# Optimization experiments

Measured on AMD Instinct MI355X. Metric: run time of the kernel, lower is better.

The kernel has to match this reference:

```python
import jax, jax.numpy as jnp
import numpy as np

HID = 128
OUT = 64
LAYERS = 2
N_ACT, N_RS, N_RD = 100000, 20000, 50000
E_F, E_RS, E_RD, E_HRD = 1600000, 800000, 800000, 800000
NEG_SLOPE = 0.2  # PyG GATConv default


def setup_inputs() -> dict:
    key = jax.random.key(0)
    k = jax.random.split(key, 20)
    s = 1.0 / np.sqrt(HID)
    inp = {
        "x_act": jax.random.normal(k[0], (N_ACT, HID), jnp.float32),
        "x_rs": jax.random.normal(k[1], (N_RS, HID), jnp.float32),
        "x_rd": jax.random.normal(k[2], (N_RD, HID), jnp.float32),
        "ef_src": jax.random.randint(k[3], (E_F,), 0, N_ACT, jnp.int32),
        "ef_dst": jax.random.randint(k[4], (E_F,), 0, N_ACT, jnp.int32),
        "ers_src": jax.random.randint(k[5], (E_RS,), 0, N_ACT, jnp.int32),
        "ers_dst": jax.random.randint(k[6], (E_RS,), 0, N_RS, jnp.int32),
        "erd_src": jax.random.randint(k[7], (E_RD,), 0, N_RD, jnp.int32),
        "erd_dst": jax.random.randint(k[8], (E_RD,), 0, N_RD, jnp.int32),
        "ehrd_src": jax.random.randint(k[9], (E_HRD,), 0, N_ACT, jnp.int32),
        "ehrd_dst": jax.random.randint(k[10], (E_HRD,), 0, N_RD, jnp.int32),
        # GAT params stacked [n_rel=4, layers=2, ...]; rel order: follows, has_rs, rd_delta, has_rd
        "Wsrc": jax.random.normal(k[11], (4, LAYERS, HID, HID), jnp.float32) * s,
        "Wdst": jax.random.normal(k[12], (4, LAYERS, HID, HID), jnp.float32) * s,
        "att_src": jax.random.normal(k[13], (4, LAYERS, HID), jnp.float32) * s,
        "att_dst": jax.random.normal(k[14], (4, LAYERS, HID), jnp.float32) * s,
        "b_gat": jnp.zeros((4, LAYERS, HID), jnp.float32),
        "W_ln": jax.random.normal(k[15], (HID, HID), jnp.float32) * s,
        "b_ln": jnp.zeros((HID,), jnp.float32),
        "W_fc": jax.random.normal(k[16], (HID, OUT), jnp.float32) * s,
        "b_fc": jnp.zeros((OUT,), jnp.float32),
    }
    return inp


def _gat(x_src, x_dst, src, dst, Ws, Wd, a_s, a_d, b):
    """Single-head PyG GATConv (add_self_loops=False), bipartite."""
    n_dst = x_dst.shape[0]
    hs = x_src @ Ws                       # [Nsrc, HID]
    hd = x_dst @ Wd                       # [Ndst, HID]
    e = jax.nn.leaky_relu((hs @ a_s)[src] + (hd @ a_d)[dst], NEG_SLOPE)  # [E]
    m = jax.ops.segment_max(e, dst, num_segments=n_dst)
    m = jnp.where(jnp.isfinite(m), m, 0.0)  # empty segments -> harmless 0
    p = jnp.exp(e - m[dst])
    z = jax.ops.segment_sum(p, dst, num_segments=n_dst)
    w = p / jnp.maximum(z, 1e-16)[dst]    # segment softmax over incoming edges
    out = jax.ops.segment_sum(w[:, None] * hs[src], dst, num_segments=n_dst)
    return out + b


def reference(x_act, x_rs, x_rd, ef_src, ef_dst, ers_src, ers_dst, erd_src, erd_dst,
              ehrd_src, ehrd_dst, Wsrc, Wdst, att_src, att_dst, b_gat,
              W_ln, b_ln, W_fc, b_fc):
    xa, xrs, xrd = x_act, x_rs, x_rd
    for L in range(LAYERS):
        a_new = _gat(xa, xa, ef_src, ef_dst, Wsrc[0, L], Wdst[0, L],
                     att_src[0, L], att_dst[0, L], b_gat[0, L])
        rs_new = _gat(xa, xrs, ers_src, ers_dst, Wsrc[1, L], Wdst[1, L],
                      att_src[1, L], att_dst[1, L], b_gat[1, L])
        # HeteroConv aggr='sum': resource_dynamic gets two conv outputs summed
        rd_new = (_gat(xrd, xrd, erd_src, erd_dst, Wsrc[2, L], Wdst[2, L],
                       att_src[2, L], att_dst[2, L], b_gat[2, L])
                  + _gat(xa, xrd, ehrd_src, ehrd_dst, Wsrc[3, L], Wdst[3, L],
                         att_src[3, L], att_dst[3, L], b_gat[3, L]))
        xa, xrs, xrd = jax.nn.relu(a_new), jax.nn.relu(rs_new), jax.nn.relu(rd_new)
    feats = jnp.stack([jnp.mean(jax.nn.relu(x @ W_ln + b_ln), axis=0)
                       for x in (xa, xrs, xrd)])  # [3, HID]
    pooled = jnp.mean(feats, axis=0)
    return pooled @ W_fc + b_fc  # [OUT]
```

## Files before the change

### kernel.cpp

```cpp
#include <hip/hip_runtime.h>
#include <cmath>

#define HID 128

typedef __attribute__((ext_vector_type(8))) short bf16x8;
typedef __attribute__((ext_vector_type(4))) float f32x4;

__device__ inline unsigned short f2bf_rne(float f) {
  unsigned int b = __float_as_uint(f);
  return (unsigned short)((b + 0x7fffu + ((b >> 16) & 1u)) >> 16);
}
__device__ inline float bf2f(unsigned int u) { return __uint_as_float(u << 16); }

#define NDTOT 220000
#define ETOT 4000000
#define BSH 8
#define BDST 256
#define NB 860
#define EPB 16384
#define NBINBLK 245


__global__ void fill_f_kernel(float* p, float v, int n) {
  int i = blockIdx.x * 256 + threadIdx.x;
  if (i < n) p[i] = v;
}

__global__ void fill_i_kernel(int* p, int v, int n) {
  int i = blockIdx.x * 256 + threadIdx.x;
  if (i < n) p[i] = v;
}

__global__ void f2bf_kernel(const float* __restrict__ in, unsigned short* __restrict__ out,
                            int n8) {
  int i = blockIdx.x * 256 + threadIdx.x;
  if (i >= n8) return;
  const float4* p4 = reinterpret_cast<const float4*>(in) + (size_t)i * 2;
  float4 v0 = p4[0], v1 = p4[1];
  float vv[8] = {v0.x, v0.y, v0.z, v0.w, v1.x, v1.y, v1.z, v1.w};
  unsigned int r[8];
#pragma unroll
  for (int j = 0; j < 8; ++j) r[j] = f2bf_rne(vv[j]);
  uint4 o;
  o.x = r[0] | (r[1] << 16);
  o.y = r[2] | (r[3] << 16);
  o.z = r[4] | (r[5] << 16);
  o.w = r[6] | (r[7] << 16);
  reinterpret_cast<uint4*>(out)[i] = o;
}

__global__ void pack_w_kernel(const float* __restrict__ Wsrc8, const float* __restrict__ W_ln,
                              unsigned short* __restrict__ Wp) {
  int g = blockIdx.y;
  const float* W = (g < 8) ? (Wsrc8 + (size_t)g * 16384) : W_ln;
  unsigned short* op = Wp + (size_t)g * 16384;
  int o = blockIdx.x * 256 + threadIdx.x;
  if (o >= 16384) return;
  int j = o & 7;
  int lane = (o >> 3) & 63;
  int kk = (o >> 9) & 3;
  int ct = (o >> 11) & 3;
  int half = (o >> 13) & 1;
  int k = kk * 32 + ((lane >> 4) * 8) + j;
  int col = half * 64 + ct * 16 + (lane & 15);
  op[o] = f2bf_rne(W[k * 128 + col]);
}

__global__ void compute_v_kernel(const float* __restrict__ W, const float* __restrict__ a,
                                 float* __restrict__ v) {
  int g = blockIdx.x, k = threadIdx.x;
  const float* Wg = W + g * 16384;
  const float* ag = a + g * 128;
  float s = 0.f;
  for (int c = 0; c < 128; ++c) s = fmaf(Wg[k * 128 + c], ag[c], s);
  v[g * 128 + k] = s;
}

__device__ inline const float* pick_vec(int r, const float* vs, const float* vd, int L) {
  switch (r) {
    case 0: return vs + (0 + L) * 128;
    case 1: return vd + (0 + L) * 128;
    case 2: return vs + (2 + L) * 128;
    case 3: return vs + (6 + L) * 128;
    case 4: return vs + (4 + L) * 128;
    case 5: return vd + (4 + L) * 128;
    case 6: return vd + (6 + L) * 128;
    default: return vd + (2 + L) * 128;
  }
}

__global__ __launch_bounds__(256) void matvec_fused_kernel(
    const unsigned short* __restrict__ xa, const unsigned short* __restrict__ xrd,
    const unsigned short* __restrict__ xrs, const float* __restrict__ vs,
    const float* __restrict__ vd, int L, float* __restrict__ af_s, float* __restrict__ af_d,
    float* __restrict__ ars_s, float* __restrict__ ahrd_s, float* __restrict__ ard_s,
    float* __restrict__ ard_d, float* __restrict__ ahrd_d, float* __restrict__ ars_d) {
  __shared__ float vl[11][128];
  int tid = threadIdx.x;
  for (int i = tid; i < 1024; i += 256) {
    int r = i >> 7;
    vl[r][i & 127] = pick_vec(r, vs, vd, L)[i & 127];
  }
  for (int i = tid; i < 384; i += 256) vl[8 + (i >> 7)][i & 127] = 0.f;
  __syncthreads();
  int wave = tid >> 6, lane = tid & 63;
  int sub = lane >> 4, li = lane & 15;
  int row = blockIdx.x * 16 + wave * 4 + sub;
  if (row >= 170000) return;
  const unsigned short* X; int lrow, vbase;
  if (row < 100000)      { X = xa;  lrow = row;          vbase = 0; }
  else if (row < 150000) { X = xrd; lrow = row - 100000; vbase = 4; }
  else                   { X = xrs; lrow = row - 150000; vbase = 7; }
  const uint4 xv = *reinterpret_cast<const uint4*>(X + (size_t)lrow * 128 + li * 8);
  float f[8];
  f[0] = bf2f(xv.x & 0xffffu); f[1] = bf2f(xv.x >> 16);
  f[2] = bf2f(xv.y & 0xffffu); f[3] = bf2f(xv.y >> 16);
  f[4] = bf2f(xv.z & 0xffffu); f[5] = bf2f(xv.z >> 16);
  f[6] = bf2f(xv.w & 0xffffu); f[7] = bf2f(xv.w >> 16);
  float a0 = 0.f, a1 = 0.f, a2 = 0.f, a3 = 0.f;
#pragma unroll
  for (int q = 0; q < 8; ++q) {
    int col = li * 8 + q;
    a0 = fmaf(f[q], vl[vbase][col], a0);
    a1 = fmaf(f[q], vl[vbase + 1][col], a1);
    a2 = fmaf(f[q], vl[vbase + 2][col], a2);
    a3 = fmaf(f[q], vl[vbase + 3][col], a3);
  }
#pragma unroll
  for (int off = 8; off >= 1; off >>= 1) {
    a0 += __shfl_xor(a0, off);
    a1 += __shfl_xor(a1, off);
    a2 += __shfl_xor(a2, off);
    a3 += __shfl_xor(a3, off);
  }
  if (li == 0) {
    if (row < 100000) {
      af_s[lrow] = a0; af_d[lrow] = a1; ars_s[lrow] = a2; ahrd_s[lrow] = a3;
    } else if (row < 150000) {
      ard_s[lrow] = a0; ard_d[lrow] = a1; ahrd_d[lrow] = a2;
    } else {
      ars_d[lrow] = a0;
    }
  }
}

__global__ void max4_kernel(const float* __restrict__ a0, const float* __restrict__ a1,
                            const float* __restrict__ a2, const float* __restrict__ a3,
                            int n0, int n1, int n2, int n3, unsigned int* __restrict__ outm) {
  int y = blockIdx.y;
  const float* a = (y == 0) ? a0 : (y == 1) ? a1 : (y == 2) ? a2 : a3;
  int n = (y == 0) ? n0 : (y == 1) ? n1 : (y == 2) ? n2 : n3;
  float m = 0.f;
  for (int i = blockIdx.x * 256 + threadIdx.x; i < n; i += gridDim.x * 256)
    m = fmaxf(m, fabsf(a[i]));
#pragma unroll
  for (int off = 32; off >= 1; off >>= 1) m = fmaxf(m, __shfl_xor(m, off));
  if ((threadIdx.x & 63) == 0) atomicMax(&outm[y], __float_as_uint(m));
}


__device__ inline void decode_edge(int e, const int* __restrict__ s0, const int* __restrict__ d0,
                                   const int* __restrict__ s1, const int* __restrict__ d1,
                                   const int* __restrict__ s2, const int* __restrict__ d2,
                                   const int* __restrict__ s3, const int* __restrict__ d3,
                                   int& src, int& gd) {
  const int* sp; const int* dp; int base, doff;
  if (e < 1600000)      { sp = s0; dp = d0; base = 0;       doff = 0; }
  else if (e < 2400000) { sp = s1; dp = d1; base = 1600000; doff = 100000; }
  else if (e < 3200000) { sp = s2; dp = d2; base = 2400000; doff = 120000; }
  else                  { sp = s3; dp = d3; base = 3200000; doff = 170000; }
  int i = e - base;
  src = sp[i];
  gd = doff + dp[i];
}

__global__ __launch_bounds__(256) void bin_hist_kernel(
    const int* __restrict__ d0, const int* __restrict__ d1, const int* __restrict__ d2,
    const int* __restrict__ d3, int* __restrict__ bcnt) {
  __shared__ int lh[NB];
  for (int i = threadIdx.x; i < NB; i += 256) lh[i] = 0;
  __syncthreads();
  int e0 = blockIdx.x * EPB;
  for (int i = 0; i < EPB; i += 256) {
    int e = e0 + i + threadIdx.x;
    if (e < ETOT) {
      const int* dp; int base, doff;
      if (e < 1600000)      { dp = d0; base = 0;       doff = 0; }
      else if (e < 2400000) { dp = d1; base = 1600000; doff = 100000; }
      else if (e < 3200000) { dp = d2; base = 2400000; doff = 120000; }
      else                  { dp = d3; base = 3200000; doff = 170000; }
      atomicAdd(&lh[(doff + dp[e - base]) >> BSH], 1);
    }
  }
  __syncthreads();
  for (int i = threadIdx.x; i < NB; i += 256)
    if (lh[i]) atomicAdd(&bcnt[i], lh[i]);
}

__global__ void scan_nb_kernel(const int* __restrict__ bcnt, int* __restrict__ bbase) {
  if (threadIdx.x == 0 && blockIdx.x == 0) {
    int run = 0;
    for (int b = 0; b < NB; ++b) { bbase[b] = run; run += bcnt[b]; }
    bbase[NB] = run;
  }
}

__global__ __launch_bounds__(256) void bin_scatter_kernel(
    const int* __restrict__ s0, const int* __restrict__ d0, const int* __restrict__ s1,
    const int* __restrict__ d1, const int* __restrict__ s2, const int* __restrict__ d2,
    const int* __restrict__ s3, const int* __restrict__ d3, const int* __restrict__ bbase,
    int* __restrict__ bfill, int2* __restrict__ pair_buf) {
  __shared__ int lh[NB];
  __shared__ int lbase[NB];
  for (int i = threadIdx.x; i < NB; i += 256) lh[i] = 0;
  __syncthreads();
  int e0 = blockIdx.x * EPB;
  for (int i = 0; i < EPB; i += 256) {
    int e = e0 + i + threadIdx.x;
    if (e < ETOT) {
      const int* dp; int base, doff;
      if (e < 1600000)      { dp = d0; base = 0;       doff = 0; }
      else if (e < 2400000) { dp = d1; base = 1600000; doff = 100000; }
      else if (e < 3200000) { dp = d2; base = 2400000; doff = 120000; }
      else                  { dp = d3; base = 3200000; doff = 170000; }
      atomicAdd(&lh[(doff + dp[e - base]) >> BSH], 1);
    }
  }
  __syncthreads();
  for (int i = threadIdx.x; i < NB; i += 256) {
    int c = lh[i];
    if (c) lbase[i] = bbase[i] + atomicAdd(&bfill[i], c);
    lh[i] = 0;
  }
  __syncthreads();
  for (int i = 0; i < EPB; i += 256) {
    int e = e0 + i + threadIdx.x;
    if (e < ETOT) {
      int src, gd;
      decode_edge(e, s0, d0, s1, d1, s2, d2, s3, d3, src, gd);
      int b = gd >> BSH;
      int pos = atomicAdd(&lh[b], 1);
      pair_buf[lbase[b] + pos] = make_int2(src, gd);
    }
  }
}

__global__ __launch_bounds__(256) void bucket_build_kernel(
    const int2* __restrict__ pair_buf, const int* __restrict__ bbase,
    int* __restrict__ rowptr_cat, int* __restrict__ csr_cat) {
  __shared__ int lcnt[BDST];
  __shared__ int lrp[BDST + 1];
  int b = blockIdx.x;
  int d0 = b << BSH;
  int nd = min(BDST, NDTOT - d0);
  int base = bbase[b], end = bbase[b + 1];
  for (int i = threadIdx.x; i < nd; i += 256) lcnt[i] = 0;
  __syncthreads();
  for (int j = base + threadIdx.x; j < end; j += 256)
    atomicAdd(&lcnt[pair_buf[j].y - d0], 1);
  __syncthreads();
  if (threadIdx.x == 0) {
    int run = base;
    for (int i = 0; i < nd; ++i) { lrp[i] = run; run += lcnt[i]; }
    lrp[nd] = run;
  }
  __syncthreads();
  for (int i = threadIdx.x; i <= nd; i += 256) rowptr_cat[d0 + i] = lrp[i];
  for (int i = threadIdx.x; i < nd; i += 256) lcnt[i] = 0;
  __syncthreads();
  for (int j = base + threadIdx.x; j < end; j += 256) {
    int2 pr = pair_buf[j];
    int ld = pr.y - d0;
    int pos = lrp[ld] + atomicAdd(&lcnt[ld], 1);
    csr_cat[pos] = pr.x;
  }
}

#define ACC8(xv, wgt)                                   \
  do {                                                  \
    a[0] = fmaf(wgt, bf2f((xv).x & 0xffffu), a[0]);     \
    a[1] = fmaf(wgt, bf2f((xv).x >> 16), a[1]);         \
    a[2] = fmaf(wgt, bf2f((xv).y & 0xffffu), a[2]);     \
    a[3] = fmaf(wgt, bf2f((xv).y >> 16), a[3]);         \
    a[4] = fmaf(wgt, bf2f((xv).z & 0xffffu), a[4]);     \
    a[5] = fmaf(wgt, bf2f((xv).z >> 16), a[5]);         \
    a[6] = fmaf(wgt, bf2f((xv).w & 0xffffu), a[6]);     \
    a[7] = fmaf(wgt, bf2f((xv).w >> 16), a[7]);         \
  } while (0)

__global__ __launch_bounds__(256) void gat_aggr_fused(
    const int* __restrict__ rowptr_cat, const int* __restrict__ csr_cat,
    const float* __restrict__ af_s, const float* __restrict__ af_d,
    const float* __restrict__ ars_s, const float* __restrict__ ars_d,
    const float* __restrict__ ard_s, const float* __restrict__ ard_d,
    const float* __restrict__ ahrd_s, const float* __restrict__ ahrd_d,
    const unsigned int* __restrict__ asmax, const unsigned short* __restrict__ xa,
    const unsigned short* __restrict__ xrd, unsigned short* __restrict__ aggh) {
  __shared__ float2 sp[4][64];
  int wave = threadIdx.x >> 6, lane = threadIdx.x & 63;
  int g = lane >> 4, li = lane & 15;
  int gd = blockIdx.x * 4 + wave;
  if (gd >= NDTOT) return;
  const float* as_; const float* ad_; const unsigned short* Xh; int midx, d;
  if (gd < 100000)      { as_ = af_s;  ad_ = af_d;  Xh = xa;  midx = 0; d = gd; }
  else if (gd < 120000) { as_ = ars_s; ad_ = ars_d; Xh = xa;  midx = 1; d = gd - 100000; }
  else if (gd < 170000) { as_ = ard_s; ad_ = ard_d; Xh = xrd; midx = 3; d = gd - 120000; }
  else                  { as_ = ahrd_s; ad_ = ahrd_d; Xh = xa; midx = 2; d = gd - 170000; }
  int beg = rowptr_cat[gd], end = rowptr_cat[gd + 1];
  float ad = ad_[d];
  float t0 = __uint_as_float(asmax[midx]) + ad;
  float mh = t0 > 0.f ? t0 : 0.2f * t0;
  float z = 0.f;
  float a[8] = {};
  for (int c0 = beg; c0 < end; c0 += 64) {
    int j = c0 + lane;
    int s = 0;
    float p = 0.f;
    if (j < end) {
      s = csr_cat[j];
      float t = as_[s] + ad;
      float e = t > 0.f ? t : 0.2f * t;
      p = __expf(e - mh);
      z += p;
    }
    sp[wave][lane] = make_float2(__int_as_float(s), p);
    asm volatile("s_waitcnt lgkmcnt(0)" ::: "memory");
    int cnt = min(64, end - c0);
    for (int k = g; k < cnt; k += 16) {
      float2 w0 = sp[wave][k];
      float2 w1 = (k + 4 < cnt) ? sp[wave][k + 4] : make_float2(0.f, 0.f);
      float2 w2 = (k + 8 < cnt) ? sp[wave][k + 8] : make_float2(0.f, 0.f);
      float2 w3 = (k + 12 < cnt) ? sp[wave][k + 12] : make_float2(0.f, 0.f);
      const uint4 x0 = *reinterpret_cast<const uint4*>(
          Xh + (size_t)(unsigned)__float_as_int(w0.x) * 128 + li * 8);
      const uint4 x1 = *reinterpret_cast<const uint4*>(
          Xh + (size_t)(unsigned)__float_as_int(w1.x) * 128 + li * 8);
      const uint4 x2 = *reinterpret_cast<const uint4*>(
          Xh + (size_t)(unsigned)__float_as_int(w2.x) * 128 + li * 8);
      const uint4 x3 = *reinterpret_cast<const uint4*>(
          Xh + (size_t)(unsigned)__float_as_int(w3.x) * 128 + li * 8);
      ACC8(x0, w0.y);
      ACC8(x1, w1.y);
      ACC8(x2, w2.y);
      ACC8(x3, w3.y);
    }
  }
#pragma unroll
  for (int off = 32; off >= 1; off >>= 1) z += __shfl_xor(z, off);
#pragma unroll
  for (int i = 0; i < 8; ++i) {
    a[i] += __shfl_xor(a[i], 32);
    a[i] += __shfl_xor(a[i], 16);
  }
  if (g == 0) {
    float inv = 1.f / fmaxf(z, 1e-16f);
    uint4 o;
    o.x = (unsigned)f2bf_rne(a[0] * inv) | ((unsigned)f2bf_rne(a[1] * inv) << 16);
    o.y = (unsigned)f2bf_rne(a[2] * inv) | ((unsigned)f2bf_rne(a[3] * inv) << 16);
    o.z = (unsigned)f2bf_rne(a[4] * inv) | ((unsigned)f2bf_rne(a[5] * inv) << 16);
    o.w = (unsigned)f2bf_rne(a[6] * inv) | ((unsigned)f2bf_rne(a[7] * inv) << 16);
    *reinterpret_cast<uint4*>(aggh + (size_t)gd * 128 + li * 8) = o;
  }
}

__global__ __launch_bounds__(256) void gemm_all_kernel(
    const unsigned short* __restrict__ aggh, const unsigned short* __restrict__ wpack,
    const float* __restrict__ b_gat, int L, unsigned short* __restrict__ ya,
    unsigned short* __restrict__ yrs, unsigned short* __restrict__ yrd) {
  int bx = blockIdx.x;
  const unsigned short *X1, *X2 = nullptr, *Wp1, *Wp2 = nullptr;
  const float *bias1, *bias2 = nullptr;
  unsigned short* Y;
  int N, r0;
  if (bx < 782) {
    int gg = 0 + L;
    X1 = aggh; Wp1 = wpack + (size_t)gg * 16384; bias1 = b_gat + gg * 128;
    Y = ya; N = 100000; r0 = bx * 128;
  } else if (bx < 939) {
    int gg = 2 + L;
    X1 = aggh + (size_t)100000 * 128; Wp1 = wpack + (size_t)gg * 16384;
    bias1 = b_gat + gg * 128;
    Y = yrs; N = 20000; r0 = (bx - 782) * 128;
  } else {
    int g2 = 4 + L, g3 = 6 + L;
    X1 = aggh + (size_t)120000 * 128; Wp1 = wpack + (size_t)g2 * 16384;
    bias1 = b_gat + g2 * 128;
    X2 = aggh + (size_t)170000 * 128; Wp2 = wpack + (size_t)g3 * 16384;
    bias2 = b_gat + g3 * 128;
    Y = yrd; N = 50000; r0 = (bx - 939) * 128;
  }
  int wid = threadIdx.x >> 6, lane = threadIdx.x & 63;
  int half = blockIdx.y;
  int rr0 = r0 + wid * 32;
  int lr = lane & 15, gk = lane >> 4;
  f32x4 acc[2][4];
#pragma unroll
  for (int rt = 0; rt < 2; ++rt)
#pragma unroll
    for (int ct = 0; ct < 4; ++ct) acc[rt][ct] = (f32x4){0.f, 0.f, 0.f, 0.f};
  int row0 = rr0 + lr, row1 = rr0 + 16 + lr;
  int nph = X2 ? 2 : 1;
  for (int ph = 0; ph < nph; ++ph) {
    const unsigned short* X = ph ? X2 : X1;
    const unsigned short* Wp = ph ? Wp2 : Wp1;
    bf16x8 b[4][4];
#pragma unroll
    for (int ct = 0; ct < 4; ++ct)
#pragma unroll
      for (int kk = 0; kk < 4; ++kk)
        b[ct][kk] = *reinterpret_cast<const bf16x8*>(Wp + ((((half * 4 + ct) * 4 + kk) * 64 + lane) << 3));
#pragma unroll
    for (int kk = 0; kk < 4; ++kk) {
      bf16x8 a0 = {}, a1 = {};
      if (row0 < N) a0 = *reinterpret_cast<const bf16x8*>(X + (size_t)row0 * 128 + kk * 32 + gk * 8);
      if (row1 < N) a1 = *reinterpret_cast<const bf16x8*>(X + (size_t)row1 * 128 + kk * 32 + gk * 8);
#pragma unroll
      for (int ct = 0; ct < 4; ++ct) {
        acc[0][ct] = __builtin_amdgcn_mfma_f32_16x16x32_bf16(a0, b[ct][kk], acc[0][ct], 0, 0, 0);
        acc[1][ct] = __builtin_amdgcn_mfma_f32_16x16x32_bf16(a1, b[ct][kk], acc[1][ct], 0, 0, 0);
      }
    }
  }
#pragma unroll
  for (int rt = 0; rt < 2; ++rt)
#pragma unroll
    for (int ct = 0; ct < 4; ++ct) {
      int col = half * 64 + ct * 16 + lr;
      float bcol = bias1[col] + (bias2 ? bias2[col] : 0.f);
#pragma unroll
      for (int reg = 0; reg < 4; ++reg) {
        int row = rr0 + rt * 16 + gk * 4 + reg;
        if (row < N) {
          float o = acc[rt][ct][reg] + bcol;
          Y[(size_t)row * 128 + col] = f2bf_rne(fmaxf(o, 0.f));
        }
      }
    }
}

__global__ __launch_bounds__(256) void head_fused_kernel(
    const unsigned short* __restrict__ xa, const unsigned short* __restrict__ xrs,
    const unsigned short* __restrict__ xrd, const unsigned short* __restrict__ Wp,
    const float* __restrict__ bias, float* __restrict__ feat) {
  __shared__ float cs[64];
  int bx = blockIdx.x;
  const unsigned short* X; float* f; int N, bx0;
  if (bx < 196)      { X = xa;  f = feat;       N = 100000; bx0 = bx; }
  else if (bx < 236) { X = xrs; f = feat + 128; N = 20000;  bx0 = bx - 196; }
  else               { X = xrd; f = feat + 256; N = 50000;  bx0 = bx - 236; }
  int wid = threadIdx.x >> 6, lane = threadIdx.x & 63;
  int half = blockIdx.y;
  int lr = lane & 15, gk = lane >> 4;
  if (threadIdx.x < 64) cs[threadIdx.x] = 0.f;
  __syncthreads();
  bf16x8 b[4][4];
#pragma unroll
  for (int ct = 0; ct < 4; ++ct)
#pragma unroll
    for (int kk = 0; kk < 4; ++kk)
      b[ct][kk] = *reinterpret_cast<const bf16x8*>(Wp + ((((half * 4 + ct) * 4 + kk) * 64 + lane) << 3));
  float colsum[4] = {0.f, 0.f, 0.f, 0.f};
  for (int c = 0; c < 4; ++c) {
    int r0 = bx0 * 512 + c * 128 + wid * 32;
    if (r0 >= N) break;
    f32x4 acc[2][4];
#pragma unroll
    for (int rt = 0; rt < 2; ++rt)
#pragma unroll
      for (int ct = 0; ct < 4; ++ct) acc[rt][ct] = (f32x4){0.f, 0.f, 0.f, 0.f};
    int row0 = r0 + lr, row1 = r0 + 16 + lr;
#pragma unroll
    for (int kk = 0; kk < 4; ++kk) {
      bf16x8 a0 = {}, a1 = {};
      if (row0 < N) a0 = *reinterpret_cast<const bf16x8*>(X + (size_t)row0 * 128 + kk * 32 + gk * 8);
      if (row1 < N) a1 = *reinterpret_cast<const bf16x8*>(X + (size_t)row1 * 128 + kk * 32 + gk * 8);
#pragma unroll
      for (int ct = 0; ct < 4; ++ct) {
        acc[0][ct] = __builtin_amdgcn_mfma_f32_16x16x32_bf16(a0, b[ct][kk], acc[0][ct], 0, 0, 0);
        acc[1][ct] = __builtin_amdgcn_mfma_f32_16x16x32_bf16(a1, b[ct][kk], acc[1][ct], 0, 0, 0);
      }
    }
#pragma unroll
    for (int rt = 0; rt < 2; ++rt)
#pragma unroll
      for (int ct = 0; ct < 4; ++ct) {
        float bcol = bias[half * 64 + ct * 16 + lr];
#pragma unroll
        for (int reg = 0; reg < 4; ++reg) {
          int row = r0 + rt * 16 + gk * 4 + reg;
          if (row < N) colsum[ct] += fmaxf(acc[rt][ct][reg] + bcol, 0.f);
        }
      }
  }
#pragma unroll
  for (int ct = 0; ct < 4; ++ct) {
    float v = colsum[ct];
    v += __shfl_xor(v, 16);
    v += __shfl_xor(v, 32);
    if (gk == 0) atomicAdd(&cs[ct * 16 + lr], v);
  }
  __syncthreads();
  if (threadIdx.x < 64) atomicAdd(&f[half * 64 + threadIdx.x], cs[threadIdx.x]);
}

__global__ void final_fc_kernel(const float* __restrict__ fa, const float* __restrict__ frs,
                                const float* __restrict__ frd, const float* __restrict__ Wfc,
                                const float* __restrict__ bfc, float* __restrict__ out) {
  __shared__ float pooled[128];
  int t = threadIdx.x;
  if (t < 128)
    pooled[t] = (fa[t] * (1.f / 100000.f) + frs[t] * (1.f / 20000.f) + frd[t] * (1.f / 50000.f)) *
                (1.f / 3.f);
  __syncthreads();
  if (t < 64) {
    float s = bfc[t];
    for (int c = 0; c < 128; ++c) s = fmaf(pooled[c], Wfc[c * 64 + t], s);
    out[t] = s;
  }
}


extern "C" void kernel_launch(void* const* d_in, const int* in_sizes, int n_in,
                              void* d_out, int out_size, void* d_ws, size_t ws_size,
                              hipStream_t stream) {
  const int N_ACT = 100000, N_RS = 20000, N_RD = 50000;

  const float* x_act = (const float*)d_in[0];
  const float* x_rs = (const float*)d_in[1];
  const float* x_rd = (const float*)d_in[2];
  const int* ef_src = (const int*)d_in[3];
  const int* ef_dst = (const int*)d_in[4];
  const int* ers_src = (const int*)d_in[5];
  const int* ers_dst = (const int*)d_in[6];
  const int* erd_src = (const int*)d_in[7];
  const int* erd_dst = (const int*)d_in[8];
  const int* ehrd_src = (const int*)d_in[9];
  const int* ehrd_dst = (const int*)d_in[10];
  const float* Wsrc = (const float*)d_in[11];
  const float* Wdst = (const float*)d_in[12];
  const float* att_src = (const float*)d_in[13];
  const float* att_dst = (const float*)d_in[14];
  const float* b_gat = (const float*)d_in[15];
  const float* W_ln = (const float*)d_in[16];
  const float* b_ln = (const float*)d_in[17];
  const float* W_fc = (const float*)d_in[18];
  const float* b_fc = (const float*)d_in[19];
  float* out = (float*)d_out;

  float* w = (float*)d_ws;
  float* af_s = w;   w += N_ACT;
  float* af_d = w;   w += N_ACT;
  float* ars_s = w;  w += N_ACT;
  float* ahrd_s = w; w += N_ACT;
  float* ard_s = w;  w += N_RD;
  float* ard_d = w;  w += N_RD;
  float* ahrd_d = w; w += N_RD;
  float* ars_d = w;  w += N_RS;
  float* vs = w;    w += 1024;
  float* vd = w;    w += 1024;
  float* feats = w; w += 384;
  unsigned int* asmax_u = (unsigned int*)w; w += 16;
  unsigned short* xa0 = (unsigned short*)w;   w += (size_t)N_ACT * 64;
  unsigned short* xa1 = (unsigned short*)w;   w += (size_t)N_ACT * 64;
  unsigned short* xrd0 = (unsigned short*)w;  w += (size_t)N_RD * 64;
  unsigned short* xrd1 = (unsigned short*)w;  w += (size_t)N_RD * 64;
  unsigned short* xrs_b = (unsigned short*)w; w += (size_t)N_RS * 64;
  unsigned short* aggh = (unsigned short*)w;  w += (size_t)NDTOT * 64;
  unsigned short* wpack = (unsigned short*)w; w += (9 * 16384) / 2;
  int* ip = (int*)w;
  int2* pair_buf = (int2*)ip; ip += 2 * ETOT;
  int* csr_cat = ip;          ip += ETOT;
  int* rowptr_cat = ip;       ip += NDTOT + 1;
  int* bcnt = ip;             ip += NB;
  int* bfill = ip;            ip += NB;
  int* bbase = ip;            ip += NB + 1;

  fill_i_kernel<<<(2 * NB + 255) / 256, 256, 0, stream>>>(bcnt, 0, 2 * NB);
  bin_hist_kernel<<<NBINBLK, 256, 0, stream>>>(ef_dst, ers_dst, erd_dst, ehrd_dst, bcnt);
  scan_nb_kernel<<<1, 64, 0, stream>>>(bcnt, bbase);
  bin_scatter_kernel<<<NBINBLK, 256, 0, stream>>>(
      ef_src, ef_dst, ers_src, ers_dst, erd_src, erd_dst, ehrd_src, ehrd_dst,
      bbase, bfill, pair_buf);
  bucket_build_kernel<<<NB, 256, 0, stream>>>(pair_buf, bbase, rowptr_cat, csr_cat);

  compute_v_kernel<<<8, 128, 0, stream>>>(Wsrc, att_src, vs);
  compute_v_kernel<<<8, 128, 0, stream>>>(Wdst, att_dst, vd);
  pack_w_kernel<<<dim3(64, 9), 256, 0, stream>>>(Wsrc, W_ln, wpack);
  f2bf_kernel<<<(N_ACT * 16 + 255) / 256, 256, 0, stream>>>(x_act, xa0, N_ACT * 16);
  f2bf_kernel<<<(N_RS * 16 + 255) / 256, 256, 0, stream>>>(x_rs, xrs_b, N_RS * 16);
  f2bf_kernel<<<(N_RD * 16 + 255) / 256, 256, 0, stream>>>(x_rd, xrd0, N_RD * 16);

  const unsigned short* xa = xa0;
  unsigned short* xa_nxt = xa1;
  const unsigned short* xrd = xrd0;
  unsigned short* xrd_nxt = xrd1;

  for (int L = 0; L < 2; ++L) {
    matvec_fused_kernel<<<(170000 + 15) / 16, 256, 0, stream>>>(
        xa, xrd, xrs_b, vs, vd, L, af_s, af_d, ars_s, ahrd_s, ard_s, ard_d, ahrd_d, ars_d);

    fill_i_kernel<<<1, 64, 0, stream>>>((int*)asmax_u, 0, 16);
    max4_kernel<<<dim3(32, 4), 256, 0, stream>>>(af_s, ars_s, ahrd_s, ard_s,
                                                 N_ACT, N_ACT, N_ACT, N_RD, asmax_u);

    gat_aggr_fused<<<(NDTOT + 3) / 4, 256, 0, stream>>>(
        rowptr_cat, csr_cat, af_s, af_d, ars_s, ars_d, ard_s, ard_d, ahrd_s, ahrd_d,
        asmax_u, xa, xrd, aggh);

    gemm_all_kernel<<<dim3(1330, 2), 256, 0, stream>>>(aggh, wpack, b_gat, L,
                                                       xa_nxt, xrs_b, xrd_nxt);

    const unsigned short* t1 = xa; xa = xa_nxt; xa_nxt = (unsigned short*)t1;
    const unsigned short* t2 = xrd; xrd = xrd_nxt; xrd_nxt = (unsigned short*)t2;
  }

  fill_f_kernel<<<2, 256, 0, stream>>>(feats, 0.f, 384);
  head_fused_kernel<<<dim3(334, 2), 256, 0, stream>>>(xa, xrs_b, xrd,
                                                      wpack + (size_t)8 * 16384, b_ln, feats);
  final_fc_kernel<<<1, 128, 0, stream>>>(feats, feats + 128, feats + 256, W_fc, b_fc, out);
}
```

Measured before the change: 624.9 us.

## Merge small setup kernels and unroll GAT aggregation with packed FMA

Several small launches are merged: the three bf16 conversions become one kernel, the two attention-vector kernels become one 2D launch, and the max-reduction now also zeroes feats, which removes the separate fill launches. The max kernel changes from 128 blocks with atomics to 4 blocks with float4 loads and a shared-memory reduction, so each block has more serial work. The aggregation loop is unrolled to 8 gathers per iteration. It uses byte-offset indices pre-shifted by 8, reads padded zero entries in shared memory instead of bounds checks, and accumulates with v_pk_fma_f32 inline asm to raise memory-level parallelism and cut ALU instructions.

```diff
diff --git a/kernel.cpp b/kernel.cpp
--- a/kernel.cpp
+++ b/kernel.cpp
@@ -5,6 +5,7 @@
 
 typedef __attribute__((ext_vector_type(8))) short bf16x8;
 typedef __attribute__((ext_vector_type(4))) float f32x4;
+typedef __attribute__((ext_vector_type(2))) float f32x2;
 
 __device__ inline unsigned short f2bf_rne(float f) {
   unsigned int b = __float_as_uint(f);
@@ -21,21 +22,21 @@
 #define NBINBLK 245
 
 
-__global__ void fill_f_kernel(float* p, float v, int n) {
-  int i = blockIdx.x * 256 + threadIdx.x;
-  if (i < n) p[i] = v;
-}
-
 __global__ void fill_i_kernel(int* p, int v, int n) {
   int i = blockIdx.x * 256 + threadIdx.x;
   if (i < n) p[i] = v;
 }
 
-__global__ void f2bf_kernel(const float* __restrict__ in, unsigned short* __restrict__ out,
-                            int n8) {
+__global__ void f2bf_all_kernel(const float* __restrict__ xa, const float* __restrict__ xrs,
+                                const float* __restrict__ xrd, unsigned short* __restrict__ oa,
+                                unsigned short* __restrict__ ors, unsigned short* __restrict__ ord) {
   int i = blockIdx.x * 256 + threadIdx.x;
-  if (i >= n8) return;
-  const float4* p4 = reinterpret_cast<const float4*>(in) + (size_t)i * 2;
+  const float* in; unsigned short* out; int li;
+  if (i < 1600000)      { in = xa;  out = oa;  li = i; }
+  else if (i < 1920000) { in = xrs; out = ors; li = i - 1600000; }
+  else if (i < 2720000) { in = xrd; out = ord; li = i - 1920000; }
+  else return;
+  const float4* p4 = reinterpret_cast<const float4*>(in) + (size_t)li * 2;
   float4 v0 = p4[0], v1 = p4[1];
   float vv[8] = {v0.x, v0.y, v0.z, v0.w, v1.x, v1.y, v1.z, v1.w};
   unsigned int r[8];
@@ -46,7 +47,7 @@
   o.y = r[2] | (r[3] << 16);
   o.z = r[4] | (r[5] << 16);
   o.w = r[6] | (r[7] << 16);
-  reinterpret_cast<uint4*>(out)[i] = o;
+  reinterpret_cast<uint4*>(out)[li] = o;
 }
 
 __global__ void pack_w_kernel(const float* __restrict__ Wsrc8, const float* __restrict__ W_ln,
@@ -66,14 +67,16 @@
   op[o] = f2bf_rne(W[k * 128 + col]);
 }
 
-__global__ void compute_v_kernel(const float* __restrict__ W, const float* __restrict__ a,
-                                 float* __restrict__ v) {
+__global__ void compute_v2_kernel(const float* __restrict__ Wsrc, const float* __restrict__ Wdst,
+                                  const float* __restrict__ as_, const float* __restrict__ ad_,
+                                  float* __restrict__ vs, float* __restrict__ vd) {
   int g = blockIdx.x, k = threadIdx.x;
-  const float* Wg = W + g * 16384;
-  const float* ag = a + g * 128;
+  const float* W = (blockIdx.y ? Wdst : Wsrc) + g * 16384;
+  const float* a = (blockIdx.y ? ad_ : as_) + g * 128;
+  float* v = (blockIdx.y ? vd : vs) + g * 128;
   float s = 0.f;
-  for (int c = 0; c < 128; ++c) s = fmaf(Wg[k * 128 + c], ag[c], s);
-  v[g * 128 + k] = s;
+  for (int c = 0; c < 128; ++c) s = fmaf(W[k * 128 + c], a[c], s);
+  v[k] = s;
 }
 
 __device__ inline const float* pick_vec(int r, const float* vs, const float* vd, int L) {
@@ -144,18 +147,29 @@
   }
 }
 
-__global__ void max4_kernel(const float* __restrict__ a0, const float* __restrict__ a1,
-                            const float* __restrict__ a2, const float* __restrict__ a3,
-                            int n0, int n1, int n2, int n3, unsigned int* __restrict__ outm) {
-  int y = blockIdx.y;
+__global__ __launch_bounds__(256) void max4_kernel(
+    const float* __restrict__ a0, const float* __restrict__ a1, const float* __restrict__ a2,
+    const float* __restrict__ a3, int n0, int n1, int n2, int n3,
+    unsigned int* __restrict__ outm, float* feats_zero) {
+  __shared__ float red[256];
+  int y = blockIdx.x, tid = threadIdx.x;
+  if (feats_zero && y == 0)
+    for (int i = tid; i < 384; i += 256) feats_zero[i] = 0.f;
   const float* a = (y == 0) ? a0 : (y == 1) ? a1 : (y == 2) ? a2 : a3;
-  int n = (y == 0) ? n0 : (y == 1) ? n1 : (y == 2) ? n2 : n3;
+  int n4 = ((y == 0) ? n0 : (y == 1) ? n1 : (y == 2) ? n2 : n3) >> 2;
   float m = 0.f;
-  for (int i = blockIdx.x * 256 + threadIdx.x; i < n; i += gridDim.x * 256)
-    m = fmaxf(m, fabsf(a[i]));
-#pragma unroll
-  for (int off = 32; off >= 1; off >>= 1) m = fmaxf(m, __shfl_xor(m, off));
-  if ((threadIdx.x & 63) == 0) atomicMax(&outm[y], __float_as_uint(m));
+  const float4* a4 = reinterpret_cast<const float4*>(a);
+  for (int i = tid; i < n4; i += 256) {
+    float4 v = a4[i];
+    m = fmaxf(m, fmaxf(fmaxf(fabsf(v.x), fabsf(v.y)), fmaxf(fabsf(v.z), fabsf(v.w))));
+  }
+  red[tid] = m;
+  __syncthreads();
+  for (int off = 128; off; off >>= 1) {
+    if (tid < off) red[tid] = fmaxf(red[tid], red[tid + off]);
+    __syncthreads();
+  }
+  if (tid == 0) outm[y] = __float_as_uint(red[0]);
 }
 
 
@@ -276,16 +290,17 @@
   }
 }
 
-#define ACC8(xv, wgt)                                   \
-  do {                                                  \
-    a[0] = fmaf(wgt, bf2f((xv).x & 0xffffu), a[0]);     \
-    a[1] = fmaf(wgt, bf2f((xv).x >> 16), a[1]);         \
-    a[2] = fmaf(wgt, bf2f((xv).y & 0xffffu), a[2]);     \
-    a[3] = fmaf(wgt, bf2f((xv).y >> 16), a[3]);         \
-    a[4] = fmaf(wgt, bf2f((xv).z & 0xffffu), a[4]);     \
-    a[5] = fmaf(wgt, bf2f((xv).z >> 16), a[5]);         \
-    a[6] = fmaf(wgt, bf2f((xv).w & 0xffffu), a[6]);     \
-    a[7] = fmaf(wgt, bf2f((xv).w >> 16), a[7]);         \
+#define ACCP(xv, wgt)                                                                \
+  do {                                                                               \
+    f32x2 wv = {wgt, wgt};                                                           \
+    f32x2 t0 = {__uint_as_float((xv).x << 16), __uint_as_float((xv).x & 0xFFFF0000u)};\
+    f32x2 t1 = {__uint_as_float((xv).y << 16), __uint_as_float((xv).y & 0xFFFF0000u)};\
+    f32x2 t2 = {__uint_as_float((xv).z << 16), __uint_as_float((xv).z & 0xFFFF0000u)};\
+    f32x2 t3 = {__uint_as_float((xv).w << 16), __uint_as_float((xv).w & 0xFFFF0000u)};\
+    asm("v_pk_fma_f32 %0, %1, %2, %0" : "+v"(a2[0]) : "v"(wv), "v"(t0));             \
+    asm("v_pk_fma_f32 %0, %1, %2, %0" : "+v"(a2[1]) : "v"(wv), "v"(t1));             \
+    asm("v_pk_fma_f32 %0, %1, %2, %0" : "+v"(a2[2]) : "v"(wv), "v"(t2));             \
+    asm("v_pk_fma_f32 %0, %1, %2, %0" : "+v"(a2[3]) : "v"(wv), "v"(t3));             \
   } while (0)
 
 __global__ __launch_bounds__(256) void gat_aggr_fused(
@@ -296,7 +311,7 @@
     const float* __restrict__ ahrd_s, const float* __restrict__ ahrd_d,
     const unsigned int* __restrict__ asmax, const unsigned short* __restrict__ xa,
     const unsigned short* __restrict__ xrd, unsigned short* __restrict__ aggh) {
-  __shared__ float2 sp[4][64];
+  __shared__ float2 sp[4][96];
   int wave = threadIdx.x >> 6, lane = threadIdx.x & 63;
   int g = lane >> 4, li = lane & 15;
   int gd = blockIdx.x * 4 + wave;
@@ -306,45 +321,57 @@
   else if (gd < 120000) { as_ = ars_s; ad_ = ars_d; Xh = xa;  midx = 1; d = gd - 100000; }
   else if (gd < 170000) { as_ = ard_s; ad_ = ard_d; Xh = xrd; midx = 3; d = gd - 120000; }
   else                  { as_ = ahrd_s; ad_ = ahrd_d; Xh = xa; midx = 2; d = gd - 170000; }
+  if (lane < 32) sp[wave][64 + lane] = make_float2(0.f, 0.f);
+  const char* Xb = reinterpret_cast<const char*>(Xh) + li * 16;
   int beg = rowptr_cat[gd], end = rowptr_cat[gd + 1];
   float ad = ad_[d];
-  float t0 = __uint_as_float(asmax[midx]) + ad;
-  float mh = t0 > 0.f ? t0 : 0.2f * t0;
+  float t0v = __uint_as_float(asmax[midx]) + ad;
+  float mh = t0v > 0.f ? t0v : 0.2f * t0v;
   float z = 0.f;
-  float a[8] = {};
+  f32x2 a2[4] = {{0.f, 0.f}, {0.f, 0.f}, {0.f, 0.f}, {0.f, 0.f}};
   for (int c0 = beg; c0 < end; c0 += 64) {
     int j = c0 + lane;
-    int s = 0;
+    int s8 = 0;
     float p = 0.f;
     if (j < end) {
-      s = csr_cat[j];
+      int s = csr_cat[j];
       float t = as_[s] + ad;
       float e = t > 0.f ? t : 0.2f * t;
       p = __expf(e - mh);
       z += p;
-    }
-    sp[wave][lane] = make_float2(__int_as_float(s), p);
+      s8 = s << 8;
+    }
+    sp[wave][lane] = make_float2(__int_as_float(s8), p);
     asm volatile("s_waitcnt lgkmcnt(0)" ::: "memory");
     int cnt = min(64, end - c0);
-    for (int k = g; k < cnt; k += 16) {
+    for (int k = g; k < cnt; k += 32) {
       float2 w0 = sp[wave][k];
-      float2 w1 = (k + 4 < cnt) ? sp[wave][k + 4] : make_float2(0.f, 0.f);
-      float2 w2 = (k + 8 < cnt) ? sp[wave][k + 8] : make_float2(0.f, 0.f);
-      float2 w3 = (k + 12 < cnt) ? sp[wave][k + 12] : make_float2(0.f, 0.f);
-      const uint4 x0 = *reinterpret_cast<const uint4*>(
-          Xh + (size_t)(unsigned)__float_as_int(w0.x) * 128 + li * 8);
-      const uint4 x1 = *reinterpret_cast<const uint4*>(
-          Xh + (size_t)(unsigned)__float_as_int(w1.x) * 128 + li * 8);
-      const uint4 x2 = *reinterpret_cast<const uint4*>(
-          Xh + (size_t)(unsigned)__float_as_int(w2.x) * 128 + li * 8);
-      const uint4 x3 = *reinterpret_cast<const uint4*>(
-          Xh + (size_t)(unsigned)__float_as_int(w3.x) * 128 + li * 8);
-      ACC8(x0, w0.y);
-      ACC8(x1, w1.y);
-      ACC8(x2, w2.y);
-      ACC8(x3, w3.y);
-    }
-  }
+      float2 w1 = sp[wave][k + 4];
+      float2 w2 = sp[wave][k + 8];
+      float2 w3 = sp[wave][k + 12];
+      float2 w4 = sp[wave][k + 16];
+      float2 w5 = sp[wave][k + 20];
+      float2 w6 = sp[wave][k + 24];
+      float2 w7 = sp[wave][k + 28];
+      const uint4 x0 = *reinterpret_cast<const uint4*>(Xb + (unsigned)__float_as_int(w0.x));
+      const uint4 x1 = *reinterpret_cast<const uint4*>(Xb + (unsigned)__float_as_int(w1.x));
+      const uint4 x2 = *reinterpret_cast<const uint4*>(Xb + (unsigned)__float_as_int(w2.x));
+      const uint4 x3 = *reinterpret_cast<const uint4*>(Xb + (unsigned)__float_as_int(w3.x));
+      const uint4 x4 = *reinterpret_cast<const uint4*>(Xb + (unsigned)__float_as_int(w4.x));
+      const uint4 x5 = *reinterpret_cast<const uint4*>(Xb + (unsigned)__float_as_int(w5.x));
+      const uint4 x6 = *reinterpret_cast<const uint4*>(Xb + (unsigned)__float_as_int(w6.x));
+      const uint4 x7 = *reinterpret_cast<const uint4*>(Xb + (unsigned)__float_as_int(w7.x));
+      ACCP(x0, w0.y);
+      ACCP(x1, w1.y);
+      ACCP(x2, w2.y);
+      ACCP(x3, w3.y);
+      ACCP(x4, w4.y);
+      ACCP(x5, w5.y);
+      ACCP(x6, w6.y);
+      ACCP(x7, w7.y);
+    }
+  }
+  float a[8] = {a2[0].x, a2[0].y, a2[1].x, a2[1].y, a2[2].x, a2[2].y, a2[3].x, a2[3].y};
 #pragma unroll
   for (int off = 32; off >= 1; off >>= 1) z += __shfl_xor(z, off);
 #pragma unroll
@@ -583,12 +610,10 @@
       bbase, bfill, pair_buf);
   bucket_build_kernel<<<NB, 256, 0, stream>>>(pair_buf, bbase, rowptr_cat, csr_cat);
 
-  compute_v_kernel<<<8, 128, 0, stream>>>(Wsrc, att_src, vs);
-  compute_v_kernel<<<8, 128, 0, stream>>>(Wdst, att_dst, vd);
+  compute_v2_kernel<<<dim3(8, 2), 128, 0, stream>>>(Wsrc, Wdst, att_src, att_dst, vs, vd);
   pack_w_kernel<<<dim3(64, 9), 256, 0, stream>>>(Wsrc, W_ln, wpack);
-  f2bf_kernel<<<(N_ACT * 16 + 255) / 256, 256, 0, stream>>>(x_act, xa0, N_ACT * 16);
-  f2bf_kernel<<<(N_RS * 16 + 255) / 256, 256, 0, stream>>>(x_rs, xrs_b, N_RS * 16);
-  f2bf_kernel<<<(N_RD * 16 + 255) / 256, 256, 0, stream>>>(x_rd, xrd0, N_RD * 16);
+  f2bf_all_kernel<<<(2720000 + 255) / 256, 256, 0, stream>>>(x_act, x_rs, x_rd,
+                                                             xa0, xrs_b, xrd0);
 
   const unsigned short* xa = xa0;
   unsigned short* xa_nxt = xa1;
@@ -599,9 +624,9 @@
     matvec_fused_kernel<<<(170000 + 15) / 16, 256, 0, stream>>>(
         xa, xrd, xrs_b, vs, vd, L, af_s, af_d, ars_s, ahrd_s, ard_s, ard_d, ahrd_d, ars_d);
 
-    fill_i_kernel<<<1, 64, 0, stream>>>((int*)asmax_u, 0, 16);
-    max4_kernel<<<dim3(32, 4), 256, 0, stream>>>(af_s, ars_s, ahrd_s, ard_s,
-                                                 N_ACT, N_ACT, N_ACT, N_RD, asmax_u);
+    max4_kernel<<<4, 256, 0, stream>>>(af_s, ars_s, ahrd_s, ard_s,
+                                       N_ACT, N_ACT, N_ACT, N_RD, asmax_u,
+                                       (L == 1) ? feats : nullptr);
 
     gat_aggr_fused<<<(NDTOT + 3) / 4, 256, 0, stream>>>(
         rowptr_cat, csr_cat, af_s, af_d, ars_s, ars_d, ard_s, ard_d, ahrd_s, ahrd_d,
@@ -614,7 +639,6 @@
     const unsigned short* t2 = xrd; xrd = xrd_nxt; xrd_nxt = (unsigned short*)t2;
   }
 
-  fill_f_kernel<<<2, 256, 0, stream>>>(feats, 0.f, 384);
   head_fused_kernel<<<dim3(334, 2), 256, 0, stream>>>(xa, xrs_b, xrd,
                                                       wpack + (size_t)8 * 16384, b_ln, feats);
   final_fc_kernel<<<1, 128, 0, stream>>>(feats, feats + 128, feats + 256, W_fc, b_fc, out);
```

Measured after the change: 682.0 us. 9.2% more time.
